# Kernel tuning notes

Hardware: AMD Instinct MI355X
Metric: run time of the kernel (lower is better)

Reference implementation:

```python
import jax, jax.numpy as jnp
import numpy as np

B, T, D, U = 64, 512, 64, 256


def setup_inputs() -> dict:
    key = jax.random.key(0)
    k1, k2, k3, k4 = jax.random.split(key, 4)
    s = 0.05
    return {
        "x": jax.random.normal(k1, (B, T, D), dtype=jnp.float32),
        "W": jax.random.normal(k2, (D, 4 * U), dtype=jnp.float32) * s,
        "U": jax.random.normal(k3, (U, 4 * U), dtype=jnp.float32) * s,
        "b": jnp.zeros((4 * U,), dtype=jnp.float32),
        "dense_w": jax.random.normal(k4, (U, 1), dtype=jnp.float32) * s,
        "dense_b": jnp.zeros((1,), dtype=jnp.float32),
    }


def reference(x, W, U, b, dense_w, dense_b):
    # Keras LSTM with activation='relu', recurrent_activation='sigmoid'.
    # Gate packing order: i, f, c(g), o.
    units = U.shape[0]
    # Precompute input projections for all timesteps: [T, B, 4U]
    xz = jnp.einsum("btd,dg->tbg", x, W) + b

    def step(carry, xz_t):
        h, c = carry
        z = xz_t + h @ U  # [B, 4U]
        i = jax.nn.sigmoid(z[:, :units])
        f = jax.nn.sigmoid(z[:, units:2 * units])
        g = jax.nn.relu(z[:, 2 * units:3 * units])
        o = jax.nn.sigmoid(z[:, 3 * units:])
        c_new = f * c + i * g
        h_new = o * jax.nn.relu(c_new)
        return (h_new, c_new), h_new

    bsz = x.shape[0]
    h0 = jnp.zeros((bsz, units), dtype=x.dtype)
    c0 = jnp.zeros((bsz, units), dtype=x.dtype)
    _, hs = jax.lax.scan(step, (h0, c0), xz)  # hs: [T, B, U]
    hs = jnp.transpose(hs, (1, 0, 2))  # [B, T, U]
    sigma = jnp.squeeze(hs @ dense_w + dense_b, axis=-1)  # [B, T]
    return sigma
```

## Files before the change

### kernel.cpp

```cpp
#include <hip/hip_runtime.h>

#define B_  64
#define T_  512
#define D_  64
#define U_  256
#define G4  1024
#define NT  512

typedef _Float16 f16x8 __attribute__((ext_vector_type(8)));
typedef float    f32x4 __attribute__((ext_vector_type(4)));

__device__ __forceinline__ float sigmoidf_(float z) {
    return 1.f / (1.f + __expf(-z));
}

__device__ __forceinline__ f16x8 load_bfrag(const float* __restrict__ Um,
                                            int ntg, int kt, int gg, int li) {
    const float* p = Um + (size_t)(32 * kt + 8 * gg) * G4 + 16 * ntg + li;
    f16x8 v;
    #pragma unroll
    for (int e = 0; e < 8; ++e) v[e] = (_Float16)p[(size_t)e * G4];
    return v;
}

#define NTGW(W, NL) (16 * ((NL) >> 1) + 2 * (W) + ((NL) & 1))

__global__ __launch_bounds__(256) void xz_kernel(const float* __restrict__ x,
                                                 const float* __restrict__ W,
                                                 const float* __restrict__ bias,
                                                 float* __restrict__ xz) {
    __shared__ float xt[16][D_];
    const int g    = blockIdx.x * 256 + threadIdx.x;
    const int row0 = blockIdx.y * 16;

    #pragma unroll
    for (int j = 0; j < 4; ++j) {
        int e = threadIdx.x + 256 * j;
        int r = e >> 6, d = e & 63;
        int row = row0 + r;
        int t = row >> 6, bb = row & 63;
        xt[r][d] = x[((size_t)bb * T_ + t) * D_ + d];
    }
    __syncthreads();

    float acc[16];
    #pragma unroll
    for (int r = 0; r < 16; ++r) acc[r] = 0.f;

    for (int d = 0; d < D_; ++d) {
        float wv = W[(size_t)d * G4 + g];
        #pragma unroll
        for (int r = 0; r < 16; ++r) acc[r] += xt[r][d] * wv;
    }

    float bg = bias[g];
    #pragma unroll
    for (int r = 0; r < 16; ++r)
        xz[(size_t)(row0 + r) * G4 + g] = acc[r] + bg;
}

__global__ __launch_bounds__(256) void pack_kernel(const float* __restrict__ Um,
                                                   f16x8* __restrict__ pk) {
    const int idx  = blockIdx.x * 256 + threadIdx.x;
    const int lane = idx & 63;
    const int fid  = idx >> 6;
    const int nl   = fid & 7;
    const int kt   = (fid >> 3) & 7;
    const int w    = fid >> 6;
    const int gg   = (lane >> 4) & 3;
    const int li   = lane & 15;
    pk[idx] = load_bfrag(Um, NTGW(w, nl), kt, gg, li);
}


struct SmemWL {
    _Float16 h16[2][256];
    float    pd[2][U_];
    f16x8    bl[8][17][64];
};

#define MMV(N, BV) acc##N = __builtin_amdgcn_mfma_f32_16x16x32_f16(av, (BV), acc##N, 0, 0, 0);
#define MMS(K, N)  { f16x8 bv = pkp[(((K) << 3) | (N)) << 6]; \
                     acc##N = __builtin_amdgcn_mfma_f32_16x16x32_f16(av, bv, acc##N, 0, 0, 0); }

#define MKLDS(KT, FB) { \
    f16x8 av = *(const f16x8*)&hp[32 * (KT) + 8 * gg]; \
    { f16x8 bv = sm.bl[w][(FB)+0][lane]; MMV(0, bv) } \
    { f16x8 bv = sm.bl[w][(FB)+1][lane]; MMV(1, bv) } \
    { f16x8 bv = sm.bl[w][(FB)+2][lane]; MMV(2, bv) } \
    { f16x8 bv = sm.bl[w][(FB)+3][lane]; MMV(3, bv) } \
    { f16x8 bv = sm.bl[w][(FB)+4][lane]; MMV(4, bv) } \
    { f16x8 bv = sm.bl[w][(FB)+5][lane]; MMV(5, bv) } \
    { f16x8 bv = sm.bl[w][(FB)+6][lane]; MMV(6, bv) } \
    { f16x8 bv = sm.bl[w][(FB)+7][lane]; MMV(7, bv) } }

#define MKSTRM(KT) { \
    f16x8 av = *(const f16x8*)&hp[32 * (KT) + 8 * gg]; \
    MMS(KT,0) MMS(KT,1) MMS(KT,2) MMS(KT,3) \
    MMS(KT,4) MMS(KT,5) MMS(KT,6) MMS(KT,7) }

__global__
__attribute__((amdgpu_flat_work_group_size(NT, NT), amdgpu_waves_per_eu(2, 2)))
void lstm_kernel(
        const float* __restrict__ Um,
        const float* __restrict__ dw,
        const float* __restrict__ dbp,
        const float* __restrict__ xz,
        const f16x8* __restrict__ pk,
        float* __restrict__ out) {
    __shared__ SmemWL sm;

    const int tau  = threadIdx.x;
    const int b    = blockIdx.x;
    const int w    = tau >> 6;
    const int lane = tau & 63;
    const int gg   = (tau >> 4) & 3;
    const int li   = tau & 15;
    const int sel  = (lane >> 4) & 1;
    const int u    = 32 * w + 16 * sel + li;

    const f16x8* __restrict__ pkp = pk + ((size_t)w << 12) + lane;

    #pragma unroll
    for (int f = 0; f < 17; ++f) {
        const int kt = (f < 8) ? 0 : (f < 16) ? 1 : 2;
        const int nl = (f < 16) ? (f & 7) : (f - 16);
        sm.bl[w][f][lane] = load_bfrag(Um, NTGW(w, nl), kt, gg, li);
    }

    if (tau < U_) sm.h16[0][tau] = (_Float16)0.f;

    const float dwr = (lane < 32) ? dw[u] : 0.f;
    const float db0 = dbp[0];
    float c_state = 0.f;

    __syncthreads();

    for (int t = 0; t < T_; ++t) {
        const int cur = t & 1, nxt = cur ^ 1;

        if (t > 0 && tau < 64) {
            const float* pp = sm.pd[nxt];
            float s = pp[tau] + pp[tau + 64] + pp[tau + 128] + pp[tau + 192];
            #pragma unroll
            for (int off = 32; off > 0; off >>= 1)
                s += __shfl_down(s, off);
            if (tau == 0) out[(size_t)b * T_ + (t - 1)] = s + db0;
        }

        float xq0 = 0.f, xq1 = 0.f, xq2 = 0.f, xq3 = 0.f;
        if (lane < 32) {
            const float* xp = xz + ((size_t)t * B_ + b) * G4;
            xq0 = xp[u];
            xq1 = xp[256 + u];
            xq2 = xp[512 + u];
            xq3 = xp[768 + u];
        }
        __builtin_amdgcn_sched_barrier(0);

        const _Float16* hp = &sm.h16[cur][0];
        f32x4 acc0 = {0.f,0.f,0.f,0.f}, acc1 = {0.f,0.f,0.f,0.f};
        f32x4 acc2 = {0.f,0.f,0.f,0.f}, acc3 = {0.f,0.f,0.f,0.f};
        f32x4 acc4 = {0.f,0.f,0.f,0.f}, acc5 = {0.f,0.f,0.f,0.f};
        f32x4 acc6 = {0.f,0.f,0.f,0.f}, acc7 = {0.f,0.f,0.f,0.f};

        MKLDS(0, 0)
        MKLDS(1, 8)
        {
            f16x8 av = *(const f16x8*)&hp[64 + 8 * gg];
            { f16x8 bv = sm.bl[w][16][lane]; MMV(0, bv) }
            MMS(2,1) MMS(2,2) MMS(2,3) MMS(2,4) MMS(2,5) MMS(2,6) MMS(2,7)
        }
        MKSTRM(3) MKSTRM(4) MKSTRM(5) MKSTRM(6) MKSTRM(7)

        if (lane < 32) {
            float zi = (sel ? acc1[0] : acc0[0]) + xq0;
            float zf = (sel ? acc3[0] : acc2[0]) + xq1;
            float zg = (sel ? acc5[0] : acc4[0]) + xq2;
            float zo = (sel ? acc7[0] : acc6[0]) + xq3;
            float ig = sigmoidf_(zi);
            float fg = sigmoidf_(zf);
            float gv = fmaxf(zg, 0.f);
            float og = sigmoidf_(zo);
            c_state = fg * c_state + ig * gv;
            float h = og * fmaxf(c_state, 0.f);
            sm.h16[nxt][u] = (_Float16)h;
            sm.pd[cur][u]  = h * dwr;
        }
        __syncthreads();
    }

    if (tau < 64) {
        const float* pp = sm.pd[(T_ - 1) & 1];
        float s = pp[tau] + pp[tau + 64] + pp[tau + 128] + pp[tau + 192];
        #pragma unroll
        for (int off = 32; off > 0; off >>= 1)
            s += __shfl_down(s, off);
        if (tau == 0) out[(size_t)b * T_ + (T_ - 1)] = s + db0;
    }
}

struct Smem15 {
    _Float16 h16[256];
    float    z[G4];
    float    pd[U_];
    f16x8    bl[8][17][64];
};

#define FOR_AG(X) \
    X(2,1) X(2,2) X(2,3) X(2,4) X(2,5) X(2,6) X(2,7) \
    X(3,0) X(3,1) X(3,2) X(3,3) X(3,4) X(3,5) X(3,6) X(3,7) \
    X(4,0) X(4,1) X(4,2) X(4,3) X(4,4) X(4,5) X(4,6) X(4,7) \
    X(5,0) X(5,1) X(5,2) X(5,3) X(5,4) X(5,5) X(5,6) X(5,7) \
    X(6,0) X(6,1) X(6,2) X(6,3) X(6,4) X(6,5) X(6,6) X(6,7) \
    X(7,0) X(7,1) X(7,2) X(7,3) X(7,4) X(7,5) X(7,6) X(7,7)

#define DB(K,N) f16x8 bF_##K##_##N;
#define IB(K,N) bF_##K##_##N = load_bfrag(Um, w8 + (N), (K), gg, li);
#define MMR(K, N)  acc##N = __builtin_amdgcn_mfma_f32_16x16x32_f16(av, bF_##K##_##N, acc##N, 0, 0, 0);
#define MKLDS15(KT, FB) { \
    f16x8 av = *(const f16x8*)&sm.h16[32 * (KT) + 8 * gg]; \
    { f16x8 bv = sm.bl[w][(FB)+0][lane]; MMV(0, bv) } \
    { f16x8 bv = sm.bl[w][(FB)+1][lane]; MMV(1, bv) } \
    { f16x8 bv = sm.bl[w][(FB)+2][lane]; MMV(2, bv) } \
    { f16x8 bv = sm.bl[w][(FB)+3][lane]; MMV(3, bv) } \
    { f16x8 bv = sm.bl[w][(FB)+4][lane]; MMV(4, bv) } \
    { f16x8 bv = sm.bl[w][(FB)+5][lane]; MMV(5, bv) } \
    { f16x8 bv = sm.bl[w][(FB)+6][lane]; MMV(6, bv) } \
    { f16x8 bv = sm.bl[w][(FB)+7][lane]; MMV(7, bv) } }
#define MKREG(KT) { \
    f16x8 av = *(const f16x8*)&sm.h16[32 * (KT) + 8 * gg]; \
    MMR(KT,0) MMR(KT,1) MMR(KT,2) MMR(KT,3) \
    MMR(KT,4) MMR(KT,5) MMR(KT,6) MMR(KT,7) }

__global__
__attribute__((amdgpu_flat_work_group_size(NT, NT), amdgpu_waves_per_eu(2, 2)))
void lstm_kernel_r15(
        const float* __restrict__ Um,
        const float* __restrict__ dw,
        const float* __restrict__ dbp,
        const float* __restrict__ xz,
        float* __restrict__ out) {
    __shared__ Smem15 sm;

    const int tau  = threadIdx.x;
    const int b    = blockIdx.x;
    const int w    = tau >> 6;
    const int lane = tau & 63;
    const int gg   = (tau >> 4) & 3;
    const int li   = tau & 15;
    const int w8   = 8 * w;

    FOR_AG(DB)
    FOR_AG(IB)
    __builtin_amdgcn_sched_barrier(0);

    #pragma unroll
    for (int f = 0; f < 17; ++f) {
        const int kt = f >> 3, nt = f & 7;
        sm.bl[w][f][lane] = load_bfrag(Um, w8 + nt, kt, gg, li);
    }

    if (tau < U_) sm.h16[tau] = (_Float16)0.f;

    const float dwr = (tau < U_) ? dw[tau] : 0.f;
    const float db0 = dbp[0];
    float c_state = 0.f;

    float xq0 = 0.f, xq1 = 0.f, xq2 = 0.f, xq3 = 0.f;
    if (tau < U_) {
        const float* xp = xz + (size_t)b * G4;
        xq0 = xp[tau]; xq1 = xp[U_ + tau]; xq2 = xp[2 * U_ + tau]; xq3 = xp[3 * U_ + tau];
    }
    __syncthreads();

    for (int t = 0; t < T_; ++t) {
        const int tn = (t + 1 < T_) ? t + 1 : t;
        float xn0 = 0.f, xn1 = 0.f, xn2 = 0.f, xn3 = 0.f;
        if (tau < U_) {
            const float* xp = xz + ((size_t)tn * B_ + b) * G4;
            xn0 = xp[tau]; xn1 = xp[U_ + tau]; xn2 = xp[2 * U_ + tau]; xn3 = xp[3 * U_ + tau];
        }
        __builtin_amdgcn_sched_barrier(0);

        f32x4 acc0 = {0.f,0.f,0.f,0.f}, acc1 = {0.f,0.f,0.f,0.f};
        f32x4 acc2 = {0.f,0.f,0.f,0.f}, acc3 = {0.f,0.f,0.f,0.f};
        f32x4 acc4 = {0.f,0.f,0.f,0.f}, acc5 = {0.f,0.f,0.f,0.f};
        f32x4 acc6 = {0.f,0.f,0.f,0.f}, acc7 = {0.f,0.f,0.f,0.f};

        MKLDS15(0, 0)
        MKLDS15(1, 8)
        {
            f16x8 av = *(const f16x8*)&sm.h16[64 + 8 * gg];
            { f16x8 bv = sm.bl[w][16][lane]; MMV(0, bv) }
            MMR(2,1) MMR(2,2) MMR(2,3) MMR(2,4) MMR(2,5) MMR(2,6) MMR(2,7)
        }
        MKREG(3) MKREG(4) MKREG(5) MKREG(6) MKREG(7)

        if (lane < 16) {
            const int zb = 128 * w + lane;
            sm.z[zb]       = acc0.x;  sm.z[zb + 16]  = acc1.x;
            sm.z[zb + 32]  = acc2.x;  sm.z[zb + 48]  = acc3.x;
            sm.z[zb + 64]  = acc4.x;  sm.z[zb + 80]  = acc5.x;
            sm.z[zb + 96]  = acc6.x;  sm.z[zb + 112] = acc7.x;
        }
        __syncthreads();

        if (tau < U_) {
            float zi = sm.z[tau]            + xq0;
            float zf = sm.z[U_ + tau]       + xq1;
            float zg = sm.z[2 * U_ + tau]   + xq2;
            float zo = sm.z[3 * U_ + tau]   + xq3;
            float ig = sigmoidf_(zi);
            float fg = sigmoidf_(zf);
            float gv = fmaxf(zg, 0.f);
            float og = sigmoidf_(zo);
            c_state = fg * c_state + ig * gv;
            float h = og * fmaxf(c_state, 0.f);
            sm.h16[tau] = (_Float16)h;
            sm.pd[tau]  = h * dwr;
        }
        __syncthreads();

        if (tau < 64) {
            float s = sm.pd[tau] + sm.pd[tau + 64] + sm.pd[tau + 128] + sm.pd[tau + 192];
            #pragma unroll
            for (int off = 32; off > 0; off >>= 1)
                s += __shfl_down(s, off);
            if (tau == 0) out[(size_t)b * T_ + t] = s + db0;
        }

        xq0 = xn0; xq1 = xn1; xq2 = xn2; xq3 = xn3;
    }
}

__global__ __launch_bounds__(1024) void lstm_fallback(
        const float* __restrict__ x,  const float* __restrict__ W,
        const float* __restrict__ Um, const float* __restrict__ bias,
        const float* __restrict__ dw, const float* __restrict__ dbp,
        float* __restrict__ out) {
    __shared__ float h_s[U_];
    __shared__ float z_s2[G4];
    __shared__ float pd_s2[U_];
    const int g = threadIdx.x;
    const int b = blockIdx.x;
    const float bg  = bias[g];
    const float dwr = (g < U_) ? dw[g] : 0.f;
    const float db0 = dbp[0];
    float c = 0.f;
    if (g < U_) h_s[g] = 0.f;
    __syncthreads();
    const float* Ucol = Um + g;
    for (int t = 0; t < T_; ++t) {
        float acc = bg;
        const float* xrow = x + ((size_t)b * T_ + t) * D_;
        for (int d = 0; d < D_; ++d) acc += xrow[d] * W[(size_t)d * G4 + g];
        for (int k = 0; k < U_; ++k) acc += h_s[k] * Ucol[(size_t)k * G4];
        z_s2[g] = acc;
        __syncthreads();
        if (g < U_) {
            float ig = sigmoidf_(z_s2[g]);
            float fg = sigmoidf_(z_s2[U_ + g]);
            float gg2 = fmaxf(z_s2[2 * U_ + g], 0.f);
            float og = sigmoidf_(z_s2[3 * U_ + g]);
            c = fg * c + ig * gg2;
            float h = og * fmaxf(c, 0.f);
            h_s[g] = h; pd_s2[g] = h * dwr;
        }
        __syncthreads();
        if (g < 64) {
            float s = pd_s2[g] + pd_s2[g + 64] + pd_s2[g + 128] + pd_s2[g + 192];
            #pragma unroll
            for (int off = 32; off > 0; off >>= 1) s += __shfl_down(s, off);
            if (g == 0) out[(size_t)b * T_ + t] = s + db0;
        }
        __syncthreads();
    }
}

extern "C" void kernel_launch(void* const* d_in, const int* in_sizes, int n_in,
                              void* d_out, int out_size, void* d_ws, size_t ws_size,
                              hipStream_t stream) {
    const float* x    = (const float*)d_in[0];
    const float* W    = (const float*)d_in[1];
    const float* Um   = (const float*)d_in[2];
    const float* bias = (const float*)d_in[3];
    const float* dw   = (const float*)d_in[4];
    const float* db   = (const float*)d_in[5];
    float* out = (float*)d_out;

    const size_t need_xz  = (size_t)T_ * B_ * G4 * sizeof(float);
    const size_t pk_bytes = (size_t)512 * 64 * 16;

    if (ws_size >= need_xz + pk_bytes) {
        f16x8* pk = (f16x8*)d_ws;
        float* xz = (float*)((char*)d_ws + pk_bytes);
        dim3 gridX(G4 / 256, (T_ * B_) / 16);
        xz_kernel<<<gridX, 256, 0, stream>>>(x, W, bias, xz);
        pack_kernel<<<128, 256, 0, stream>>>(Um, pk);
        lstm_kernel<<<B_, NT, 0, stream>>>(Um, dw, db, xz, pk, out);
    } else if (ws_size >= need_xz) {
        float* xz = (float*)d_ws;
        dim3 gridX(G4 / 256, (T_ * B_) / 16);
        xz_kernel<<<gridX, 256, 0, stream>>>(x, W, bias, xz);
        lstm_kernel_r15<<<B_, NT, 0, stream>>>(Um, dw, db, xz, out);
    } else {
        lstm_fallback<<<B_, 1024, 0, stream>>>(x, W, Um, bias, dw, db, out);
    }
}
```

Before: 839.7 us.

## Split recurrent matmul across 16 waves with per-gate column tiles

Doubles the LSTM block from 512 to 1024 threads so each of 16 waves owns 16 hidden units and computes 4 gate tiles instead of 8. The packed-weight layout, LDS cache split and gate mapping are changed to match, so each wave now does half the MFMA chain per timestep. This shortens the serial per-step critical path but adds more waves to the per-step barrier, cuts the register budget, and leaves fewer lanes active in the gate nonlinearity.

Result: slower. 1.356 ms (+61.5%).

```diff
diff --git a/kernel.cpp b/kernel.cpp
--- a/kernel.cpp
+++ b/kernel.cpp
@@ -5,7 +5,8 @@
 #define D_  64
 #define U_  256
 #define G4  1024
-#define NT  512
+#define NT  1024
+#define NLDS2 9
 
 typedef _Float16 f16x8 __attribute__((ext_vector_type(8)));
 typedef float    f32x4 __attribute__((ext_vector_type(4)));
@@ -23,7 +24,7 @@
     return v;
 }
 
-#define NTGW(W, NL) (16 * ((NL) >> 1) + 2 * (W) + ((NL) & 1))
+#define NTG16(W, Q) (16 * (Q) + (W))
 
 __global__ __launch_bounds__(256) void xz_kernel(const float* __restrict__ x,
                                                  const float* __restrict__ W,
@@ -64,43 +65,31 @@
     const int idx  = blockIdx.x * 256 + threadIdx.x;
     const int lane = idx & 63;
     const int fid  = idx >> 6;
-    const int nl   = fid & 7;
-    const int kt   = (fid >> 3) & 7;
-    const int w    = fid >> 6;
+    const int q    = fid & 3;
+    const int kt   = (fid >> 2) & 7;
+    const int w    = fid >> 5;
     const int gg   = (lane >> 4) & 3;
     const int li   = lane & 15;
-    pk[idx] = load_bfrag(Um, NTGW(w, nl), kt, gg, li);
-}
-
-
-struct SmemWL {
+    pk[idx] = load_bfrag(Um, NTG16(w, q), kt, gg, li);
+}
+
+
+struct Smem16 {
     _Float16 h16[2][256];
     float    pd[2][U_];
-    f16x8    bl[8][17][64];
+    f16x8    bl[16][NLDS2][64];
 };
 
 #define MMV(N, BV) acc##N = __builtin_amdgcn_mfma_f32_16x16x32_f16(av, (BV), acc##N, 0, 0, 0);
-#define MMS(K, N)  { f16x8 bv = pkp[(((K) << 3) | (N)) << 6]; \
-                     acc##N = __builtin_amdgcn_mfma_f32_16x16x32_f16(av, bv, acc##N, 0, 0, 0); }
-
-#define MKLDS(KT, FB) { \
+#define MMS(K, Q)  { f16x8 bv = pkp[(((K) << 2) | (Q)) << 6]; \
+                     acc##Q = __builtin_amdgcn_mfma_f32_16x16x32_f16(av, bv, acc##Q, 0, 0, 0); }
+
+#define MKSTRM4(KT) { \
     f16x8 av = *(const f16x8*)&hp[32 * (KT) + 8 * gg]; \
-    { f16x8 bv = sm.bl[w][(FB)+0][lane]; MMV(0, bv) } \
-    { f16x8 bv = sm.bl[w][(FB)+1][lane]; MMV(1, bv) } \
-    { f16x8 bv = sm.bl[w][(FB)+2][lane]; MMV(2, bv) } \
-    { f16x8 bv = sm.bl[w][(FB)+3][lane]; MMV(3, bv) } \
-    { f16x8 bv = sm.bl[w][(FB)+4][lane]; MMV(4, bv) } \
-    { f16x8 bv = sm.bl[w][(FB)+5][lane]; MMV(5, bv) } \
-    { f16x8 bv = sm.bl[w][(FB)+6][lane]; MMV(6, bv) } \
-    { f16x8 bv = sm.bl[w][(FB)+7][lane]; MMV(7, bv) } }
-
-#define MKSTRM(KT) { \
-    f16x8 av = *(const f16x8*)&hp[32 * (KT) + 8 * gg]; \
-    MMS(KT,0) MMS(KT,1) MMS(KT,2) MMS(KT,3) \
-    MMS(KT,4) MMS(KT,5) MMS(KT,6) MMS(KT,7) }
+    MMS(KT,0) MMS(KT,1) MMS(KT,2) MMS(KT,3) }
 
 __global__
-__attribute__((amdgpu_flat_work_group_size(NT, NT), amdgpu_waves_per_eu(2, 2)))
+__attribute__((amdgpu_flat_work_group_size(NT, NT), amdgpu_waves_per_eu(4, 4)))
 void lstm_kernel(
         const float* __restrict__ Um,
         const float* __restrict__ dw,
@@ -108,7 +97,7 @@
         const float* __restrict__ xz,
         const f16x8* __restrict__ pk,
         float* __restrict__ out) {
-    __shared__ SmemWL sm;
+    __shared__ Smem16 sm;
 
     const int tau  = threadIdx.x;
     const int b    = blockIdx.x;
@@ -116,21 +105,20 @@
     const int lane = tau & 63;
     const int gg   = (tau >> 4) & 3;
     const int li   = tau & 15;
-    const int sel  = (lane >> 4) & 1;
-    const int u    = 32 * w + 16 * sel + li;
-
-    const f16x8* __restrict__ pkp = pk + ((size_t)w << 12) + lane;
-
-    #pragma unroll
-    for (int f = 0; f < 17; ++f) {
-        const int kt = (f < 8) ? 0 : (f < 16) ? 1 : 2;
-        const int nl = (f < 16) ? (f & 7) : (f - 16);
-        sm.bl[w][f][lane] = load_bfrag(Um, NTGW(w, nl), kt, gg, li);
+    const int u    = 16 * w + li;
+
+    const f16x8* __restrict__ pkp = pk + ((size_t)w << 11) + lane;
+
+    #pragma unroll
+    for (int f = 0; f < NLDS2; ++f) {
+        const int kt = (f < 4) ? 0 : (f < 8) ? 1 : 2;
+        const int q  = (f < 8) ? (f & 3) : 0;
+        sm.bl[w][f][lane] = load_bfrag(Um, NTG16(w, q), kt, gg, li);
     }
 
     if (tau < U_) sm.h16[0][tau] = (_Float16)0.f;
 
-    const float dwr = (lane < 32) ? dw[u] : 0.f;
+    const float dwr = (lane < 16) ? dw[u] : 0.f;
     const float db0 = dbp[0];
     float c_state = 0.f;
 
@@ -149,7 +137,7 @@
         }
 
         float xq0 = 0.f, xq1 = 0.f, xq2 = 0.f, xq3 = 0.f;
-        if (lane < 32) {
+        if (lane < 16) {
             const float* xp = xz + ((size_t)t * B_ + b) * G4;
             xq0 = xp[u];
             xq1 = xp[256 + u];
@@ -161,23 +149,33 @@
         const _Float16* hp = &sm.h16[cur][0];
         f32x4 acc0 = {0.f,0.f,0.f,0.f}, acc1 = {0.f,0.f,0.f,0.f};
         f32x4 acc2 = {0.f,0.f,0.f,0.f}, acc3 = {0.f,0.f,0.f,0.f};
-        f32x4 acc4 = {0.f,0.f,0.f,0.f}, acc5 = {0.f,0.f,0.f,0.f};
-        f32x4 acc6 = {0.f,0.f,0.f,0.f}, acc7 = {0.f,0.f,0.f,0.f};
-
-        MKLDS(0, 0)
-        MKLDS(1, 8)
+
+        {
+            f16x8 av = *(const f16x8*)&hp[8 * gg];
+            { f16x8 bv = sm.bl[w][0][lane]; MMV(0, bv) }
+            { f16x8 bv = sm.bl[w][1][lane]; MMV(1, bv) }
+            { f16x8 bv = sm.bl[w][2][lane]; MMV(2, bv) }
+            { f16x8 bv = sm.bl[w][3][lane]; MMV(3, bv) }
+        }
+        {
+            f16x8 av = *(const f16x8*)&hp[32 + 8 * gg];
+            { f16x8 bv = sm.bl[w][4][lane]; MMV(0, bv) }
+            { f16x8 bv = sm.bl[w][5][lane]; MMV(1, bv) }
+            { f16x8 bv = sm.bl[w][6][lane]; MMV(2, bv) }
+            { f16x8 bv = sm.bl[w][7][lane]; MMV(3, bv) }
+        }
         {
             f16x8 av = *(const f16x8*)&hp[64 + 8 * gg];
-            { f16x8 bv = sm.bl[w][16][lane]; MMV(0, bv) }
-            MMS(2,1) MMS(2,2) MMS(2,3) MMS(2,4) MMS(2,5) MMS(2,6) MMS(2,7)
-        }
-        MKSTRM(3) MKSTRM(4) MKSTRM(5) MKSTRM(6) MKSTRM(7)
-
-        if (lane < 32) {
-            float zi = (sel ? acc1[0] : acc0[0]) + xq0;
-            float zf = (sel ? acc3[0] : acc2[0]) + xq1;
-            float zg = (sel ? acc5[0] : acc4[0]) + xq2;
-            float zo = (sel ? acc7[0] : acc6[0]) + xq3;
+            { f16x8 bv = sm.bl[w][8][lane]; MMV(0, bv) }
+            MMS(2,1) MMS(2,2) MMS(2,3)
+        }
+        MKSTRM4(3) MKSTRM4(4) MKSTRM4(5) MKSTRM4(6) MKSTRM4(7)
+
+        if (lane < 16) {
+            float zi = acc0[0] + xq0;
+            float zf = acc1[0] + xq1;
+            float zg = acc2[0] + xq2;
+            float zo = acc3[0] + xq3;
             float ig = sigmoidf_(zi);
             float fg = sigmoidf_(zf);
             float gv = fmaxf(zg, 0.f);
@@ -234,7 +232,7 @@
     MMR(KT,4) MMR(KT,5) MMR(KT,6) MMR(KT,7) }
 
 __global__
-__attribute__((amdgpu_flat_work_group_size(NT, NT), amdgpu_waves_per_eu(2, 2)))
+__attribute__((amdgpu_flat_work_group_size(512, 512), amdgpu_waves_per_eu(2, 2)))
 void lstm_kernel_r15(
         const float* __restrict__ Um,
         const float* __restrict__ dw,
@@ -403,7 +401,7 @@
         float* xz = (float*)d_ws;
         dim3 gridX(G4 / 256, (T_ * B_) / 16);
         xz_kernel<<<gridX, 256, 0, stream>>>(x, W, bias, xz);
-        lstm_kernel_r15<<<B_, NT, 0, stream>>>(Um, dw, db, xz, out);
+        lstm_kernel_r15<<<B_, 512, 0, stream>>>(Um, dw, db, xz, out);
     } else {
         lstm_fallback<<<B_, 1024, 0, stream>>>(x, W, Um, bias, dw, db, out);
     }
```
